# Optimization experiments

Hardware: AMD Instinct MI355X
Metric: run time of the kernel (lower is better)

Reference implementation:

```python
import jax, jax.numpy as jnp
import numpy as np
import math

EPS = 1e-5
N_HEADS = 4


def _ln(x, g, b):
    mu = jnp.mean(x, axis=-1, keepdims=True)
    var = jnp.mean((x - mu) ** 2, axis=-1, keepdims=True)
    return (x - mu) * jax.lax.rsqrt(var + EPS) * g + b


def _eq_ln(s, v, g, b, vscale):
    # scalar LayerNorm + equivariant vector norm rescaling
    s = _ln(s, g, b)
    vn = jnp.sqrt(jnp.sum(v * v, axis=-1, keepdims=True))  # (B,N,C,1)
    v = v / (vn + EPS) * jnp.mean(vn, axis=-2, keepdims=True) * vscale[None, None, :, None]
    return s, v


def _block(s, v, pos, Wq, bq, Wk, bk, Wv, bv, Wo, bo, w_dist, b_dist, Wvv, Wvo,
           g1, be1, vs1, g2, be2, vs2, Wf1, bf1, Wf2, bf2, Wfv1, Wfv2):
    B, N, S = s.shape
    D = S // N_HEADS
    # --- norm1 + attention ---
    sn, vn = _eq_ln(s, v, g1, be1, vs1)
    q = (sn @ Wq + bq).reshape(B, N, N_HEADS, D)
    k = (sn @ Wk + bk).reshape(B, N, N_HEADS, D)
    vs = (sn @ Wv + bv).reshape(B, N, N_HEADS, D)
    attn = jnp.einsum('bnhd,bmhd->bhnm', q, k) / math.sqrt(D)
    # pairwise Euclidean distance via the |x|^2 + |y|^2 - 2xy trick (clamped for sqrt safety)
    p2 = jnp.sum(pos * pos, axis=-1)  # (B,N)
    d2 = p2[:, :, None] + p2[:, None, :] - 2.0 * jnp.einsum('bnd,bmd->bnm', pos, pos)
    dist = jnp.sqrt(jnp.maximum(d2, 1e-12))  # (B,N,N)
    # dist_proj: Linear(1 -> n_heads) + Softplus, applied per pair
    bias = jax.nn.softplus(dist[..., None] * w_dist + b_dist)  # (B,N,N,H)
    attn = jax.nn.softmax(attn - jnp.transpose(bias, (0, 3, 1, 2)), axis=-1)  # (B,H,N,N)
    attn_mean = jnp.mean(attn, axis=1)  # (B,N,N)
    s_attn = jnp.einsum('bhnm,bmhd->bnhd', attn, vs).reshape(B, N, S) @ Wo + bo
    # vector channel mixing + rotation by head-averaged attention
    v_mix = jnp.einsum('bncx,ce->bnex', vn, Wvv)          # (B,N,C,3)
    v_attn = jnp.einsum('bnm,bmcx->bncx', attn_mean, v_mix)
    v_attn = jnp.einsum('bncx,ce->bnex', v_attn, Wvo)
    s = s + s_attn
    v = v + v_attn
    # --- norm2 + FFN ---
    sn, vn = _eq_ln(s, v, g2, be2, vs2)
    s = s + (jax.nn.gelu(sn @ Wf1 + bf1, approximate=False) @ Wf2 + bf2)
    v = v + jnp.einsum('bnhx,hc->bncx', jnp.einsum('bncx,ch->bnhx', vn, Wfv1), Wfv2)
    return s, v


def setup_inputs() -> dict:
    B, N, S, C, H = 4, 2048, 256, 64, N_HEADS
    key = jax.random.key(0)
    ks = jax.random.split(key, 24)

    def nrm(k, shape, scale=0.02):
        return jax.random.normal(k, shape, dtype=jnp.float32) * scale

    return {
        's': jax.random.normal(ks[0], (B, N, S), dtype=jnp.float32),
        'v': jax.random.normal(ks[1], (B, N, C, 3), dtype=jnp.float32),
        'pos': jax.random.normal(ks[2], (B, N, 3), dtype=jnp.float32),
        'Wq': nrm(ks[3], (S, S)), 'bq': nrm(ks[4], (S,)),
        'Wk': nrm(ks[5], (S, S)), 'bk': nrm(ks[6], (S,)),
        'Wv': nrm(ks[7], (S, S)), 'bv': nrm(ks[8], (S,)),
        'Wo': nrm(ks[9], (S, S)), 'bo': nrm(ks[10], (S,)),
        'w_dist': nrm(ks[11], (H,), 0.5), 'b_dist': nrm(ks[12], (H,), 0.5),
        'Wvv': nrm(ks[13], (C, C)), 'Wvo': nrm(ks[14], (C, C)),
        'g1': jnp.ones((S,), jnp.float32), 'be1': jnp.zeros((S,), jnp.float32),
        'vs1': jnp.ones((C,), jnp.float32),
        'g2': jnp.ones((S,), jnp.float32), 'be2': jnp.zeros((S,), jnp.float32),
        'vs2': jnp.ones((C,), jnp.float32),
        'Wf1': nrm(ks[15], (S, 4 * S)), 'bf1': nrm(ks[16], (4 * S,)),
        'Wf2': nrm(ks[17], (4 * S, S)), 'bf2': nrm(ks[18], (S,)),
        'Wfv1': nrm(ks[19], (C, 4 * C)), 'Wfv2': nrm(ks[20], (4 * C, C)),
    }


def reference(s, v, pos, Wq, bq, Wk, bk, Wv, bv, Wo, bo, w_dist, b_dist, Wvv, Wvo,
              g1, be1, vs1, g2, be2, vs2, Wf1, bf1, Wf2, bf2, Wfv1, Wfv2):
    return _block(s, v, pos, Wq, bq, Wk, bk, Wv, bv, Wo, bo, w_dist, b_dist, Wvv, Wvo,
                  g1, be1, vs1, g2, be2, vs2, Wf1, bf1, Wf2, bf2, Wfv1, Wfv2)
```

## Files before the change

### kernel.cpp

```cpp
#include <hip/hip_runtime.h>
#include <hip/hip_bf16.h>

using bf16 = __hip_bfloat16;
typedef __attribute__((ext_vector_type(8))) short short8;
typedef __attribute__((ext_vector_type(4))) float float4v;
typedef __attribute__((ext_vector_type(16))) float f32x16;
typedef __attribute__((ext_vector_type(4))) unsigned uint4v;

__device__ __forceinline__ float b2f(bf16 x){ return __bfloat162float(x); }
__device__ __forceinline__ bf16  f2b(float x){ return __float2bfloat16(x); }
__device__ __forceinline__ bf16  tob(float x){ return f2b(x); }
__device__ __forceinline__ bf16  tob(bf16 x){ return x; }
__device__ __forceinline__ float frcp(float x){ return __builtin_amdgcn_rcpf(x); }
__device__ __forceinline__ float bs2f(short s){
  unsigned u = ((unsigned)(unsigned short)s) << 16;
  return __builtin_bit_cast(float, u);
}
__device__ __forceinline__ unsigned cvt_pk_bf16(float lo, float hi){
  unsigned r; asm("v_cvt_pk_bf16_f32 %0, %1, %2" : "=v"(r) : "v"(lo), "v"(hi)); return r;
}
__device__ __forceinline__ void plswap(unsigned &a, unsigned &b){
  asm("v_permlane32_swap_b32 %0, %1" : "+v"(a), "+v"(b));
}

#define EPSV 1e-5f
#define Z16 {0.f,0.f,0.f,0.f,0.f,0.f,0.f,0.f,0.f,0.f,0.f,0.f,0.f,0.f,0.f,0.f}

__global__ __launch_bounds__(256) void pos_kernel(const float* __restrict__ pos,
                                                  float* __restrict__ posf, int rows){
  int r = blockIdx.x*256 + threadIdx.x;
  if (r >= rows) return;
  float x = pos[3*r], y = pos[3*r+1], z = pos[3*r+2];
  posf[4*r] = x; posf[4*r+1] = y; posf[4*r+2] = z; posf[4*r+3] = x*x + y*y + z*z;
}

struct WTDesc { const float* src; bf16* dst; int rows, cols; };
struct WTPack { WTDesc d[10]; };

__global__ __launch_bounds__(256) void wtrans_kernel(WTPack p){
  WTDesc w = p.d[blockIdx.z];
  long r0 = (long)blockIdx.y*32, c0 = (long)blockIdx.x*32;
  if (r0 >= w.rows || c0 >= w.cols) return;
  __shared__ bf16 tile[32][33];
  int tx = threadIdx.x & 31, ty = threadIdx.x >> 5;
#pragma unroll
  for (int i = ty; i < 32; i += 8) tile[i][tx] = f2b(w.src[(r0+i)*w.cols + c0 + tx]);
  __syncthreads();
#pragma unroll
  for (int i = ty; i < 32; i += 8) w.dst[(c0+i)*w.rows + r0 + tx] = tile[tx][i];
}

template<typename TI>
__global__ __launch_bounds__(256) void transpose_kernel(
    const TI* __restrict__ in, long ldin, long is1, long is2,
    bf16* __restrict__ out, long ldout, long os1, long os2, int Z2)
{
  int z = blockIdx.z, z1 = z / Z2, z2 = z - z1*Z2;
  in  += (long)z1*is1 + (long)z2*is2;
  out += (long)z1*os1 + (long)z2*os2;
  __shared__ bf16 tile[32][33];
  int tx = threadIdx.x & 31, ty = threadIdx.x >> 5;
  long r0 = (long)blockIdx.y*32, c0 = (long)blockIdx.x*32;
#pragma unroll
  for (int i = ty; i < 32; i += 8) tile[i][tx] = tob(in[(r0+i)*ldin + c0 + tx]);
  __syncthreads();
#pragma unroll
  for (int i = ty; i < 32; i += 8) out[(c0+i)*ldout + r0 + tx] = tile[tx][i];
}

__global__ __launch_bounds__(256) void bcat_kernel(const float* __restrict__ bq,
                                                   const float* __restrict__ bk,
                                                   const float* __restrict__ bv,
                                                   float* __restrict__ bqkv){
  int j = blockIdx.x*256 + threadIdx.x;
  if (j >= 768) return;
  bqkv[j] = (j < 256) ? bq[j] : (j < 512) ? bk[j-256] : bv[j-512];
}

__global__ __launch_bounds__(256) void ln_kernel(const float* __restrict__ x,
                                                 const float* __restrict__ g,
                                                 const float* __restrict__ be,
                                                 bf16* __restrict__ out){
  const long row = blockIdx.x;
  const int t = threadIdx.x;
  __shared__ float r1[256], r2[256];
  float v = x[(row<<8) + t];
  r1[t] = v; r2[t] = v*v; __syncthreads();
  for (int s=128;s>0;s>>=1){
    if (t<s){ r1[t] += r1[t+s]; r2[t] += r2[t+s]; }
    __syncthreads();
  }
  const float mu = r1[0] * (1.f/256.f);
  const float var = r2[0] * (1.f/256.f) - mu*mu;
  const float rstd = rsqrtf(fmaxf(var, 0.f) + EPSV);
  out[(row<<8)+t] = f2b((v-mu)*rstd*g[t] + be[t]);
}

__global__ __launch_bounds__(192) void vnorm1_kernel(const float* __restrict__ vin,
                                                     const float* __restrict__ vs1,
                                                     bf16* __restrict__ vnX){
  const long row = blockIdx.x;
  const int t = threadIdx.x;
  __shared__ float vv[192], nrm[64];
  __shared__ float smean;
  vv[t] = vin[row*192 + t];
  __syncthreads();
  if (t < 64){
    float a = vv[3*t], b = vv[3*t+1], c = vv[3*t+2];
    nrm[t] = sqrtf(a*a + b*b + c*c);
  }
  __syncthreads();
  if (t == 0){ float s = 0.f; for (int i=0;i<64;i++) s += nrm[i]; smean = s*(1.f/64.f); }
  __syncthreads();
  const int c = t/3, x = t - 3*c;
  const float val = vv[t] / (nrm[c] + EPSV) * smean * vs1[c];
  vnX[row*192 + x*64 + c] = f2b(val);
}

__global__ __launch_bounds__(192) void vnorm2_kernel(const float* __restrict__ v2X,
                                                     const float* __restrict__ vs2,
                                                     bf16* __restrict__ vn2X){
  const long row = blockIdx.x;
  const int t = threadIdx.x;
  __shared__ float vv[192], nrm[64];
  __shared__ float smean;
  vv[t] = v2X[row*192 + t];
  __syncthreads();
  if (t < 64){
    float a = vv[t], b = vv[t+64], c = vv[t+128];
    nrm[t] = sqrtf(a*a + b*b + c*c);
  }
  __syncthreads();
  if (t == 0){ float s = 0.f; for (int i=0;i<64;i++) s += nrm[i]; smean = s*(1.f/64.f); }
  __syncthreads();
  const int c = t & 63;
  vn2X[row*192 + t] = f2b(vv[t] / (nrm[c] + EPSV) * smean * vs2[c]);
}

__global__ __launch_bounds__(256) void knorm_kernel(const bf16* __restrict__ qkv,
                                                    float* __restrict__ kmax){
  const int bh = blockIdx.x, b = bh>>2, h = bh&3;
  const int t = threadIdx.x;
  __shared__ float red[256];
  float mx = 0.f;
  for (int r=0;r<8;r++){
    long row = (long)b*2048 + r*256 + t;
    const short8* kp = (const short8*)(qkv + row*768 + 256 + h*64);
    float ss = 0.f;
#pragma unroll
    for (int c=0;c<8;c++){
      short8 v = kp[c];
#pragma unroll
      for (int j=0;j<8;j++){ float f = bs2f(v[j]); ss = fmaf(f,f,ss); }
    }
    mx = fmaxf(mx, ss);
  }
  red[t] = mx; __syncthreads();
  for (int s=128;s>0;s>>=1){ if (t<s) red[t] = fmaxf(red[t], red[t+s]); __syncthreads(); }
  if (t==0) kmax[bh] = sqrtf(red[0]);
}

#define ATT_K_OFF   0
#define ATT_V_OFF   4096
#define ATT_X_OFF   9216
#define ATT_P_OFF   24576
#define ATT_TILE    25088
#define ATT_GRP     50176
#define ATT_LACC    98304
#define ATT_SMEM    100352

__global__ __launch_bounds__(512, 2) void attn_kernel(
    const bf16* __restrict__ qkv,
    const bf16* __restrict__ vsT,
    const bf16* __restrict__ vmixT,
    const float* __restrict__ posf,
    const float* __restrict__ kmaxA,
    const float* __restrict__ w_dist, const float* __restrict__ b_dist,
    bf16* __restrict__ sA,
    bf16* __restrict__ slab)
{
  __shared__ __align__(16) char smem[ATT_SMEM];
  const int qb = blockIdx.x;
  const int bh = blockIdx.y;
  const int b  = bh >> 2, h = bh & 3;
  const int tid = threadIdx.x;
  const int w = tid >> 6, lane = tid & 63;
  const int g = w >> 2, qw = w & 3;
  const int lq = lane & 31, hi = lane >> 5;
  const int gtid = tid & 255;

  const int qloc = qb*128 + qw*32 + lq;
  const long rowQ = (long)b*2048 + qloc;

  short8 qf[4];
  {
    const bf16* qp = qkv + rowQ*768 + h*64 + hi*8;
#pragma unroll
    for (int kc=0;kc<4;kc++) qf[kc] = *(const short8*)(qp + kc*16);
  }
  float q2 = 0.f;
#pragma unroll
  for (int kc=0;kc<4;kc++)
#pragma unroll
    for (int j=0;j<8;j++){ float qv = bs2f(qf[kc][j]); q2 = fmaf(qv,qv,q2); }
  q2 += __shfl_xor(q2, 32);
  const float mxs = sqrtf(q2) * kmaxA[bh] * 0.125f;
  const float wh = w_dist[h], bhd = b_dist[h];
  const float4v pn = *(const float4v*)(posf + (long)b*8192 + (long)qloc*4);

  f32x16 O[2]  = {Z16, Z16};
  f32x16 VM[6] = {Z16, Z16, Z16, Z16, Z16, Z16};
  float lacc = 0.f;

  short8 stK, stV, stX0, stX1, stX2; float4v stP;
  const int sm = gtid >> 3, sc = gtid & 7;
  const int vd = gtid >> 2, vc = gtid & 3;
  const bf16* Kg = qkv + (long)b*2048*768 + 256 + h*64;
  const bf16* Vg = vsT + (long)b*524288 + (long)h*131072;
  const bf16* Xg = vmixT + (long)b*393216;
  const float* Pg = posf + (long)b*8192;
  char* gbase = smem + g*ATT_GRP;

  auto LOADT = [&](int m0){
    stK  = *(const short8*)(Kg + (long)(m0+sm)*768 + sc*8);
    stV  = *(const short8*)(Vg + (long)vd*2048 + m0 + vc*8);
    stX0 = *(const short8*)(Xg + (long)vd*2048 + m0 + vc*8);
    stX1 = *(const short8*)(Xg + (long)(64+vd)*2048 + m0 + vc*8);
    stX2 = *(const short8*)(Xg + (long)(128+vd)*2048 + m0 + vc*8);
    if (gtid < 32) stP = *(const float4v*)(Pg + (long)(m0+gtid)*4);
  };
  auto WRITET = [&](char* buf){
    *(short8*)(buf + ATT_K_OFF + sm*128 + ((sc ^ (sm&7))<<4)) = stK;
    *(short8*)(buf + ATT_V_OFF + vd*80 + vc*16) = stV;
    *(short8*)(buf + ATT_X_OFF + vd*80 + vc*16) = stX0;
    *(short8*)(buf + ATT_X_OFF + (64+vd)*80 + vc*16) = stX1;
    *(short8*)(buf + ATT_X_OFF + (128+vd)*80 + vc*16) = stX2;
    if (gtid < 32) *(float4v*)(buf + ATT_P_OFF + gtid*16) = stP;
  };

  auto COMPUTE = [&](const char* buf){
    const char* Kb = buf + ATT_K_OFF;
    const char* Vb = buf + ATT_V_OFF;
    const char* Xb = buf + ATT_X_OFF;
    const float4v* pmb = (const float4v*)(buf + ATT_P_OFF);
    f32x16 S = Z16;
#pragma unroll
    for (int kc=0;kc<4;kc++){
      short8 kf = *(const short8*)(Kb + lq*128 + (((kc*2+hi) ^ (lq&7))<<4));
      S = __builtin_amdgcn_mfma_f32_32x32x16_bf16(kf, qf[kc], S, 0, 0, 0);
    }
    float P[16];
#pragma unroll
    for (int gg=0; gg<4; gg++){
#pragma unroll
      for (int i=0;i<4;i++){
        float4v pm = pmb[gg*8 + hi*4 + i];
        float d2 = pn[3] + pm[3] - 2.f*(pn[0]*pm[0] + pn[1]*pm[1] + pn[2]*pm[2]);
        float dist = sqrtf(fmaxf(d2, 1e-12f));
        float sig = frcp(1.f + __expf(fmaf(dist, wh, bhd)));
        float p = __expf(fmaf(S[gg*4+i], 0.125f, -mxs)) * sig;
        lacc += p;
        P[gg*4+i] = p;
      }
    }
    unsigned pk[8];
#pragma unroll
    for (int t=0;t<8;t++) pk[t] = cvt_pk_bf16(P[2*t], P[2*t+1]);
    plswap(pk[0], pk[2]); plswap(pk[1], pk[3]);
    plswap(pk[4], pk[6]); plswap(pk[5], pk[7]);
    uint4v y0v = {pk[0], pk[1], pk[2], pk[3]};
    uint4v y1v = {pk[4], pk[5], pk[6], pk[7]};
    short8 Y0 = __builtin_bit_cast(short8, y0v);
    short8 Y1 = __builtin_bit_cast(short8, y1v);
#pragma unroll
    for (int dblk=0; dblk<2; dblk++){
      short8 v0 = *(const short8*)(Vb + (dblk*32+lq)*80 + hi*16);
      short8 v1 = *(const short8*)(Vb + (dblk*32+lq)*80 + 32 + hi*16);
      O[dblk] = __builtin_amdgcn_mfma_f32_32x32x16_bf16(v0, Y0, O[dblk], 0,0,0);
      O[dblk] = __builtin_amdgcn_mfma_f32_32x32x16_bf16(v1, Y1, O[dblk], 0,0,0);
    }
#pragma unroll
    for (int eblk=0; eblk<6; eblk++){
      short8 x0 = *(const short8*)(Xb + (eblk*32+lq)*80 + hi*16);
      short8 x1 = *(const short8*)(Xb + (eblk*32+lq)*80 + 32 + hi*16);
      VM[eblk] = __builtin_amdgcn_mfma_f32_32x32x16_bf16(x0, Y0, VM[eblk], 0,0,0);
      VM[eblk] = __builtin_amdgcn_mfma_f32_32x32x16_bf16(x1, Y1, VM[eblk], 0,0,0);
    }
  };

  LOADT(g*32);
  WRITET(gbase);
  __syncthreads();
#pragma unroll 1
  for (int i=0; i<32; ++i){
    if (i < 31) LOADT((2*(i+1)+g)*32);
    COMPUTE(gbase + (i&1)*ATT_TILE);
    if (i < 31) WRITET(gbase + ((i+1)&1)*ATT_TILE);
    __syncthreads();
  }

  float* laccT = (float*)(smem + ATT_LACC);
  laccT[w*64 + lane] = lacc;
  if (g == 1){
    float* Od = (float*)(smem + (qw*64+lane)*128);
#pragma unroll
    for (int r=0;r<16;r++){ Od[r] = O[0][r]; Od[16+r] = O[1][r]; }
  }
  __syncthreads();
  const float lsum = laccT[qw*64+lq] + laccT[qw*64+32+lq]
                   + laccT[(4+qw)*64+lq] + laccT[(4+qw)*64+32+lq];
  if (g == 0){
    const float* Od = (const float*)(smem + (qw*64+lane)*128);
#pragma unroll
    for (int r=0;r<16;r++){ O[0][r] += Od[r]; O[1][r] += Od[16+r]; }
  }
  __syncthreads();
  if (g == 0){
    float* Vd = (float*)(smem + (qw*64+lane)*384);
#pragma unroll
    for (int e=0;e<6;e++)
#pragma unroll
      for (int r=0;r<16;r++) Vd[e*16+r] = VM[e][r];
  }
  __syncthreads();
  if (g == 1){
    const float* Vd = (const float*)(smem + (qw*64+lane)*384);
#pragma unroll
    for (int e=0;e<6;e++)
#pragma unroll
      for (int r=0;r<16;r++) VM[e][r] += Vd[e*16+r];
  }
  __syncthreads();

  const float sinv = frcp(lsum);
  if (g == 0){
    char* scr = smem + qw*12544;
#pragma unroll
    for (int dblk=0; dblk<2; dblk++)
#pragma unroll
      for (int pp=0; pp<8; pp++){
        const int r = 2*pp;
        const int d = dblk*32 + (r&3) + 8*(r>>2) + 4*hi;
        unsigned u = cvt_pk_bf16(O[dblk][r]*sinv, O[dblk][r+1]*sinv);
        *(unsigned*)(scr + lq*136 + d*2) = u;
      }
  } else {
    const float vinv = 0.25f * sinv;
    char* scr = smem + ATT_GRP + qw*12544;
#pragma unroll
    for (int eblk=0; eblk<6; eblk++)
#pragma unroll
      for (int pp=0; pp<8; pp++){
        const int r = 2*pp;
        const int e = eblk*32 + (r&3) + 8*(r>>2) + 4*hi;
        unsigned u = cvt_pk_bf16(VM[eblk][r]*vinv, VM[eblk][r+1]*vinv);
        *(unsigned*)(scr + lq*392 + e*2) = u;
      }
  }
  __syncthreads();
  if (g == 0){
    const char* scr = smem + qw*12544;
    const int q = lane >> 1, half = lane & 1;
    const char* src = scr + q*136 + half*64;
    char* dst = (char*)(sA + (long)(b*2048 + qb*128 + qw*32 + q)*256 + h*64 + half*32);
#pragma unroll
    for (int i=0;i<8;i++)
      *(unsigned long long*)(dst + i*8) = *(const unsigned long long*)(src + i*8);
  } else {
    const char* scr = smem + ATT_GRP + qw*12544;
    const int q = lane >> 1, half = lane & 1;
    const char* src = scr + q*392 + half*192;
    char* dst = (char*)(slab + (long)h*1572864
                        + (long)(b*2048 + qb*128 + qw*32 + q)*192 + half*96);
#pragma unroll
    for (int i=0;i<24;i++)
      *(unsigned long long*)(dst + i*8) = *(const unsigned long long*)(src + i*8);
  }
}

__global__ __launch_bounds__(256) void hred_kernel(const bf16* __restrict__ slab,
                                                   bf16* __restrict__ out){
  long i = (long)blockIdx.x*256 + threadIdx.x;
  if (i >= 196608) return;
  const short8* s0 = (const short8*)slab + i;
  short8 a = s0[0], b = s0[196608], c = s0[2*196608], d = s0[3*196608];
  short8 o;
#pragma unroll
  for (int j=0;j<8;j++){
    float f = bs2f(a[j]) + bs2f(b[j]) + bs2f(c[j]) + bs2f(d[j]);
    bf16 hv = f2b(f); o[j] = *(short*)&hv;
  }
  ((short8*)out)[i] = o;
}

template<int MT, int NT, int ACT, int OUTM, int RXIL, int CXIL>
__global__ __launch_bounds__(64) void gemm_kernel(
    const bf16* __restrict__ A, long lda, long As1, long As2,
    const bf16* __restrict__ BT, long ldb, long Bs1, long Bs2,
    const float* __restrict__ bias,
    const float* __restrict__ resid, long ldr, long Rs1, long Rs2,
    void* __restrict__ Cv, long ldc, long Cs1, long Cs2,
    int K, int Z2, int KS)
{
  int z = blockIdx.z;
  int zz = z / KS, ks = z - zz*KS;
  int z1 = zz / Z2, z2 = zz - z1*Z2;
  A  += (long)z1*As1 + (long)z2*As2 + (long)ks*K;
  BT += (long)z1*Bs1 + (long)z2*Bs2 + (long)ks*K;
  if (resid) resid += (long)z1*Rs1 + (long)z2*Rs2;
  const long cbase = (long)z1*Cs1 + (long)z2*Cs2;

  const int lane = threadIdx.x;
  const int col = lane & 15, quad = lane >> 4;
  const long rowA0 = (long)blockIdx.y*(16*MT);
  const long colB0 = (long)blockIdx.x*(16*NT);

  float4v acc[MT][NT];
#pragma unroll
  for (int m=0;m<MT;m++)
#pragma unroll
    for (int n=0;n<NT;n++) acc[m][n] = (float4v){0.f,0.f,0.f,0.f};

  const bf16* ap[MT];
  const bf16* bp[NT];
#pragma unroll
  for (int m=0;m<MT;m++) ap[m] = A + (rowA0 + m*16 + col)*lda + quad*8;
#pragma unroll
  for (int n=0;n<NT;n++) bp[n] = BT + (colB0 + n*16 + col)*ldb + quad*8;

  for (int k0 = 0; k0 < K; k0 += 32){
    short8 a[MT], bb[NT];
#pragma unroll
    for (int m=0;m<MT;m++){ a[m] = *(const short8*)ap[m]; ap[m] += 32; }
#pragma unroll
    for (int n=0;n<NT;n++){ bb[n] = *(const short8*)bp[n]; bp[n] += 32; }
#pragma unroll
    for (int m=0;m<MT;m++)
#pragma unroll
      for (int n=0;n<NT;n++)
        acc[m][n] = __builtin_amdgcn_mfma_f32_16x16x32_bf16(a[m], bb[n], acc[m][n], 0, 0, 0);
  }

#pragma unroll
  for (int m=0;m<MT;m++){
    const long ri = rowA0 + m*16 + quad*4;
#pragma unroll
    for (int n=0;n<NT;n++){
      const long cj = colB0 + n*16 + col;
      const float bbias = bias ? bias[cj] : 0.f;
#pragma unroll
      for (int r=0;r<4;r++){
        const long ci = ri + r;
        float val = acc[m][n][r] + bbias;
        if (ACT == 1) val = 0.5f*val*(1.f + erff(val*0.70710678118654752f));
        if (resid){
          const long raddr = RXIL ? ((ci/3)*192 + cj*3 + (ci%3)) : (ci*ldr + cj);
          val += resid[raddr];
        }
        const long caddr = CXIL ? (cbase + (ci/3)*192 + cj*3 + (ci%3))
                                : (cbase + ci*ldc + cj);
        if (OUTM == 0)      ((bf16*)Cv)[caddr] = f2b(val);
        else if (OUTM == 1) ((float*)Cv)[caddr] = val;
        else                unsafeAtomicAdd(&((float*)Cv)[caddr], val);
      }
    }
  }
}

extern "C" void kernel_launch(void* const* d_in, const int* in_sizes, int n_in,
                              void* d_out, int out_size, void* d_ws, size_t ws_size,
                              hipStream_t stream)
{
  const float* s    = (const float*)d_in[0];
  const float* v    = (const float*)d_in[1];
  const float* pos  = (const float*)d_in[2];
  const float* Wq   = (const float*)d_in[3];
  const float* bq   = (const float*)d_in[4];
  const float* Wk   = (const float*)d_in[5];
  const float* bk   = (const float*)d_in[6];
  const float* Wv   = (const float*)d_in[7];
  const float* bv   = (const float*)d_in[8];
  const float* Wo   = (const float*)d_in[9];
  const float* bo   = (const float*)d_in[10];
  const float* w_d  = (const float*)d_in[11];
  const float* b_d  = (const float*)d_in[12];
  const float* Wvv  = (const float*)d_in[13];
  const float* Wvo  = (const float*)d_in[14];
  const float* g1   = (const float*)d_in[15];
  const float* be1  = (const float*)d_in[16];
  const float* vs1  = (const float*)d_in[17];
  const float* g2   = (const float*)d_in[18];
  const float* be2  = (const float*)d_in[19];
  const float* vs2  = (const float*)d_in[20];
  const float* Wf1  = (const float*)d_in[21];
  const float* bf1  = (const float*)d_in[22];
  const float* Wf2  = (const float*)d_in[23];
  const float* bf2  = (const float*)d_in[24];
  const float* Wfv1 = (const float*)d_in[25];
  const float* Wfv2 = (const float*)d_in[26];

  float* outS = (float*)d_out;
  float* outV = outS + (size_t)4*2048*256;

  char* w = (char*)d_ws;
  size_t o = 0;
  auto alloc = [&](size_t bytes)->char* {
    char* p = w + o;
    o = (o + bytes + 255) & ~(size_t)255;
    return p;
  };
  float* posf  = (float*)alloc(131072);
  bf16* WqkvT = (bf16*)alloc(393216);
  bf16* WoT   = (bf16*)alloc(131072);
  bf16* Wf1T  = (bf16*)alloc(524288);
  bf16* Wf2T  = (bf16*)alloc(524288);
  bf16* WvvT  = (bf16*)alloc(8192);
  bf16* WvoT  = (bf16*)alloc(8192);
  bf16* Wfv1T = (bf16*)alloc(32768);
  bf16* Wfv2T = (bf16*)alloc(32768);
  float* bqkv = (float*)alloc(3072);
  float* kmax = (float*)alloc(64);
  bf16* sn    = (bf16*)alloc(4194304);
  bf16* qkv   = (bf16*)alloc(12582912);
  bf16* vsT   = (bf16*)alloc(4194304);
  bf16* sA    = (bf16*)alloc(4194304);
  float* s2   = (float*)alloc(8388608);
  bf16* vnX   = (bf16*)alloc(3145728);
  bf16* vmixX = (bf16*)alloc(3145728);
  bf16* vmixXT= (bf16*)alloc(3145728);
  float* v2X  = (float*)alloc(6291456);
  bf16* slab  = (bf16*)alloc(12582912);
  bf16* h1    = (bf16*)alloc(16777216);
  bf16* vn2X  = vnX;
  bf16* tvXb  = vmixX;
  bf16* hv    = qkv;
  if (o > ws_size) return;

  pos_kernel<<<32, 256, 0, stream>>>(pos, posf, 8192);
  WTPack pk;
  pk.d[0] = {Wq,   WqkvT,          256, 256};
  pk.d[1] = {Wk,   WqkvT + 65536,  256, 256};
  pk.d[2] = {Wv,   WqkvT + 131072, 256, 256};
  pk.d[3] = {Wo,   WoT,            256, 256};
  pk.d[4] = {Wf1,  Wf1T,           256, 1024};
  pk.d[5] = {Wf2,  Wf2T,           1024, 256};
  pk.d[6] = {Wvv,  WvvT,           64, 64};
  pk.d[7] = {Wvo,  WvoT,           64, 64};
  pk.d[8] = {Wfv1, Wfv1T,          64, 256};
  pk.d[9] = {Wfv2, Wfv2T,          256, 64};
  wtrans_kernel<<<dim3(32,32,10), 256, 0, stream>>>(pk);
  bcat_kernel<<<3, 256, 0, stream>>>(bq, bk, bv, bqkv);

  ln_kernel<<<8192, 256, 0, stream>>>(s, g1, be1, sn);
  vnorm1_kernel<<<8192, 192, 0, stream>>>(v, vs1, vnX);

  gemm_kernel<2,4,0,0,0,0><<<dim3(1,768,1), 64, 0, stream>>>(vnX,64,0,0, WvvT,64,0,0,
      nullptr, nullptr,0,0,0, vmixX,64,0,0, 64, 1, 1);
  transpose_kernel<bf16><<<dim3(6,64,4), 256, 0, stream>>>(vmixX, 192, 393216,0,
      vmixXT, 2048, 393216,0, 1);

  gemm_kernel<2,4,0,0,0,0><<<dim3(12,256,1), 64, 0, stream>>>(sn,256,0,0, WqkvT,256,0,0,
      bqkv, nullptr,0,0,0, qkv,768,0,0, 256, 1, 1);
  transpose_kernel<bf16><<<dim3(2,64,16), 256, 0, stream>>>(qkv+512, 768, 1572864,64,
      vsT, 2048, 524288,131072, 4);

  knorm_kernel<<<16, 256, 0, stream>>>(qkv, kmax);
  attn_kernel<<<dim3(16,16), 512, 0, stream>>>(qkv, vsT, vmixXT, posf, kmax,
      w_d, b_d, sA, slab);
  hred_kernel<<<768, 256, 0, stream>>>(slab, tvXb);

  gemm_kernel<2,4,0,1,0,0><<<dim3(4,256,1), 64, 0, stream>>>(sA,256,0,0, WoT,256,0,0,
      bo, s,256,0,0, s2,256,0,0, 256, 1, 1);

  gemm_kernel<2,4,0,1,1,0><<<dim3(1,768,1), 64, 0, stream>>>(tvXb,64,0,0, WvoT,64,0,0,
      nullptr, v,0,0,0, v2X,64,0,0, 64, 1, 1);

  ln_kernel<<<8192, 256, 0, stream>>>(s2, g2, be2, sn);
  gemm_kernel<2,4,1,0,0,0><<<dim3(16,256,1), 64, 0, stream>>>(sn,256,0,0, Wf1T,256,0,0,
      bf1, nullptr,0,0,0, h1,1024,0,0, 256, 1, 1);
  gemm_kernel<2,4,0,1,0,0><<<dim3(4,256,1), 64, 0, stream>>>(h1,1024,0,0, Wf2T,1024,0,0,
      bf2, s2,256,0,0, outS,256,0,0, 1024, 1, 1);

  vnorm2_kernel<<<8192, 192, 0, stream>>>(v2X, vs2, vn2X);
  gemm_kernel<2,4,0,0,0,0><<<dim3(4,768,1), 64, 0, stream>>>(vn2X,64,0,0, Wfv1T,64,0,0,
      nullptr, nullptr,0,0,0, hv,256,0,0, 64, 1, 1);
  gemm_kernel<2,4,0,1,0,1><<<dim3(1,768,1), 64, 0, stream>>>(hv,256,0,0, Wfv2T,256,0,0,
      nullptr, v2X,64,0,0, outV,0,0,0, 256, 1, 1);
}
```

Baseline: 427.5 us.

## Split attention key loop across three wave groups instead of two

The attention kernel grows from 512 to 768 threads so three 4-wave groups each stream a third of the key tiles with their own double buffer. The partial O, VM and row-sum accumulators from the three groups are merged through padded shared memory, with VM reduced in two halves to fit. Shared memory rises to about 150 KB and the grid stays at 256 blocks, so each block gets more parallel waves to hide latency, at the cost of a larger reduction and an uneven last iteration. The distance term is also rewritten as a chain of fused multiply-adds with precomputed -2*pos.

```diff
diff --git a/kernel.cpp b/kernel.cpp
--- a/kernel.cpp
+++ b/kernel.cpp
@@ -166,10 +166,10 @@
 #define ATT_P_OFF   24576
 #define ATT_TILE    25088
 #define ATT_GRP     50176
-#define ATT_LACC    98304
-#define ATT_SMEM    100352
-
-__global__ __launch_bounds__(512, 2) void attn_kernel(
+#define ATT_LACC    150528
+#define ATT_SMEM    153600
+
+__global__ __launch_bounds__(768, 3) void attn_kernel(
     const bf16* __restrict__ qkv,
     const bf16* __restrict__ vsT,
     const bf16* __restrict__ vmixT,
@@ -207,6 +207,7 @@
   const float mxs = sqrtf(q2) * kmaxA[bh] * 0.125f;
   const float wh = w_dist[h], bhd = b_dist[h];
   const float4v pn = *(const float4v*)(posf + (long)b*8192 + (long)qloc*4);
+  const float m2x = -2.f*pn[0], m2y = -2.f*pn[1], m2z = -2.f*pn[2], pnw = pn[3];
 
   f32x16 O[2]  = {Z16, Z16};
   f32x16 VM[6] = {Z16, Z16, Z16, Z16, Z16, Z16};
@@ -255,7 +256,7 @@
 #pragma unroll
       for (int i=0;i<4;i++){
         float4v pm = pmb[gg*8 + hi*4 + i];
-        float d2 = pn[3] + pm[3] - 2.f*(pn[0]*pm[0] + pn[1]*pm[1] + pn[2]*pm[2]);
+        float d2 = fmaf(m2x, pm[0], fmaf(m2y, pm[1], fmaf(m2z, pm[2], pnw + pm[3])));
         float dist = sqrtf(fmaxf(d2, 1e-12f));
         float sig = frcp(1.f + __expf(fmaf(dist, wh, bhd)));
         float p = __expf(fmaf(S[gg*4+i], 0.125f, -mxs)) * sig;
@@ -292,45 +293,57 @@
   WRITET(gbase);
   __syncthreads();
 #pragma unroll 1
-  for (int i=0; i<32; ++i){
-    if (i < 31) LOADT((2*(i+1)+g)*32);
-    COMPUTE(gbase + (i&1)*ATT_TILE);
-    if (i < 31) WRITET(gbase + ((i+1)&1)*ATT_TILE);
+  for (int i=0; i<22; ++i){
+    const int tn = 3*(i+1)+g;
+    if (tn < 64) LOADT(tn*32);
+    if (3*i+g < 64) COMPUTE(gbase + (i&1)*ATT_TILE);
+    if (tn < 64) WRITET(gbase + ((i+1)&1)*ATT_TILE);
     __syncthreads();
   }
 
   float* laccT = (float*)(smem + ATT_LACC);
   laccT[w*64 + lane] = lacc;
-  if (g == 1){
-    float* Od = (float*)(smem + (qw*64+lane)*128);
+  if (g >= 1){
+    float* Od = (float*)(smem + g*ATT_GRP) + (qw*64+lane)*33;
 #pragma unroll
     for (int r=0;r<16;r++){ Od[r] = O[0][r]; Od[16+r] = O[1][r]; }
   }
   __syncthreads();
-  const float lsum = laccT[qw*64+lq] + laccT[qw*64+32+lq]
-                   + laccT[(4+qw)*64+lq] + laccT[(4+qw)*64+32+lq];
+  float lsum = 0.f;
+#pragma unroll
+  for (int gg=0; gg<3; gg++)
+    lsum += laccT[(gg*4+qw)*64 + lq] + laccT[(gg*4+qw)*64 + 32 + lq];
   if (g == 0){
-    const float* Od = (const float*)(smem + (qw*64+lane)*128);
-#pragma unroll
-    for (int r=0;r<16;r++){ O[0][r] += Od[r]; O[1][r] += Od[16+r]; }
-  }
-  __syncthreads();
-  if (g == 0){
-    float* Vd = (float*)(smem + (qw*64+lane)*384);
-#pragma unroll
-    for (int e=0;e<6;e++)
-#pragma unroll
-      for (int r=0;r<16;r++) Vd[e*16+r] = VM[e][r];
-  }
-  __syncthreads();
-  if (g == 1){
-    const float* Vd = (const float*)(smem + (qw*64+lane)*384);
-#pragma unroll
-    for (int e=0;e<6;e++)
-#pragma unroll
-      for (int r=0;r<16;r++) VM[e][r] += Vd[e*16+r];
-  }
-  __syncthreads();
+#pragma unroll
+    for (int a=1; a<3; a++){
+      const float* Od = (const float*)(smem + a*ATT_GRP) + (qw*64+lane)*33;
+#pragma unroll
+      for (int r=0;r<16;r++){ O[0][r] += Od[r]; O[1][r] += Od[16+r]; }
+    }
+  }
+  __syncthreads();
+#pragma unroll
+  for (int hf=0; hf<2; hf++){
+    if (g != 1){
+      float* Vd = (float*)(smem + g*ATT_GRP) + (qw*64+lane)*49;
+#pragma unroll
+      for (int e=0;e<3;e++)
+#pragma unroll
+        for (int r=0;r<16;r++) Vd[e*16+r] = VM[hf*3+e][r];
+    }
+    __syncthreads();
+    if (g == 1){
+#pragma unroll
+      for (int a=0; a<3; a+=2){
+        const float* Vd = (const float*)(smem + a*ATT_GRP) + (qw*64+lane)*49;
+#pragma unroll
+        for (int e=0;e<3;e++)
+#pragma unroll
+          for (int r=0;r<16;r++) VM[hf*3+e][r] += Vd[e*16+r];
+      }
+    }
+    __syncthreads();
+  }
 
   const float sinv = frcp(lsum);
   if (g == 0){
@@ -344,7 +357,7 @@
         unsigned u = cvt_pk_bf16(O[dblk][r]*sinv, O[dblk][r+1]*sinv);
         *(unsigned*)(scr + lq*136 + d*2) = u;
       }
-  } else {
+  } else if (g == 1){
     const float vinv = 0.25f * sinv;
     char* scr = smem + ATT_GRP + qw*12544;
 #pragma unroll
@@ -366,7 +379,7 @@
 #pragma unroll
     for (int i=0;i<8;i++)
       *(unsigned long long*)(dst + i*8) = *(const unsigned long long*)(src + i*8);
-  } else {
+  } else if (g == 1){
     const char* scr = smem + ATT_GRP + qw*12544;
     const int q = lane >> 1, half = lane & 1;
     const char* src = scr + q*392 + half*192;
@@ -565,7 +578,7 @@
       vsT, 2048, 524288,131072, 4);
 
   knorm_kernel<<<16, 256, 0, stream>>>(qkv, kmax);
-  attn_kernel<<<dim3(16,16), 512, 0, stream>>>(qkv, vsT, vmixXT, posf, kmax,
+  attn_kernel<<<dim3(16,16), 768, 0, stream>>>(qkv, vsT, vmixXT, posf, kmax,
       w_d, b_d, sA, slab);
   hred_kernel<<<768, 256, 0, stream>>>(slab, tvXb);
 
```

Result: slower. 1.259 ms (+194.5%).
